# Optimization experiments

Measured on AMD Instinct MI355X. Metric: run time of the kernel, lower is better.

Reference implementation:

```python
import jax, jax.numpy as jnp
import numpy as np

N = 16384          # number of nodes
FEAT = 256         # in_features
POOL_RATIO = 0.5
K = max(2, int(POOL_RATIO * N))  # 8192, static


def setup_inputs() -> dict:
    key = jax.random.key(0)
    k1, k2, k3 = jax.random.split(key, 3)
    x = jax.random.normal(k1, (N, FEAT), dtype=jnp.float32)
    # dense proxy for the adjacency matrix (source calls A.todense())
    A = jax.random.uniform(k2, (N, N), dtype=jnp.float32)
    # fc: Linear(FEAT, 1, bias=None) -> weight vector of shape [FEAT]
    W = jax.random.normal(k3, (FEAT,), dtype=jnp.float32) * (1.0 / np.sqrt(FEAT))
    return {"x": x, "A": A, "W": W}


def reference(x, A, W):
    # score = fc(dropout(x)); dropout p=0 -> identity
    score = x @ W                                   # [N]
    # global L2 normalization: score / sqrt(sum(score**2))
    score = score / jnp.sqrt(jnp.sum(score * score))
    score = jnp.tanh(score)                         # activation_gPool
    values, idx = jax.lax.top_k(score, K)           # [K], [K]
    new_x = x[idx, :] * values[:, None]             # gather + scale  [K, FEAT]
    new_A = A[idx, :][:, idx]                       # [K, K] subgraph adjacency
    return new_x, new_A, idx
```

## Files before the change

kernel.cpp:

```cpp
#include <hip/hip_runtime.h>
#include <hip/hip_bf16.h>

#define N     16384
#define FEAT  256
#define KSEL  8192
#define NCHUNK 16
#define CHUNK (N / NCHUNK)

typedef float f32x4 __attribute__((ext_vector_type(4)));

__device__ __align__(16) double             g_s[N];
__device__ __align__(16) unsigned long long g_key[N];
__device__ __align__(16) int                g_cnt[N];
__device__ __align__(16) int                g_sel[KSEL];
__device__ __align__(16) float              g_vals[KSEL];
__device__              double              g_norminv;

static __device__ __forceinline__ unsigned long long mono_key(double s) {
    unsigned long long u = (unsigned long long)__double_as_longlong(s);
    if (u & 0x8000000000000000ull) u = ~u;
    else                           u |= 0x8000000000000000ull;
    return u;
}

__global__ __launch_bounds__(512) void k_score(const float* __restrict__ x,
                                               const float* __restrict__ W) {
    int lane = threadIdx.x & 63;
    int row  = blockIdx.x * 8 + (threadIdx.x >> 6);
    float4 xv = reinterpret_cast<const float4*>(x)[row * 64 + lane];
    float4 wv = reinterpret_cast<const float4*>(W)[lane];
    double acc = (double)xv.x * (double)wv.x + (double)xv.y * (double)wv.y
               + (double)xv.z * (double)wv.z + (double)xv.w * (double)wv.w;
    #pragma unroll
    for (int m = 32; m >= 1; m >>= 1) acc += __shfl_xor(acc, m, 64);
    if (lane == 0) { g_s[row] = acc; g_key[row] = mono_key(acc); g_cnt[row] = 0; }
}

__global__ __launch_bounds__(256) void k_rank() {
    __shared__ unsigned long long lk[CHUNK];
    int i = blockIdx.x * 256 + threadIdx.x;
    int jbase = blockIdx.y * CHUNK;
    for (int t = threadIdx.x; t < CHUNK; t += 256) lk[t] = g_key[jbase + t];
    __syncthreads();
    unsigned long long ki = g_key[i];
    int c = 0;
    #pragma unroll 8
    for (int jj = 0; jj < CHUNK; ++jj) {
        unsigned long long kj = lk[jj];
        c += (int)((kj > ki) | ((kj == ki) & ((jbase + jj) < i)));
    }
    atomicAdd(&g_cnt[i], c);

    if (blockIdx.x == 0 && blockIdx.y == 0) {
        __shared__ double red[256];
        double acc = 0.0;
        for (int j = threadIdx.x; j < N; j += 256) { double v = g_s[j]; acc += v * v; }
        red[threadIdx.x] = acc;
        __syncthreads();
        for (int w = 128; w >= 1; w >>= 1) {
            if ((int)threadIdx.x < w) red[threadIdx.x] += red[threadIdx.x + w];
            __syncthreads();
        }
        if (threadIdx.x == 0) g_norminv = 1.0 / sqrt(red[0]);
    }
}

__global__ void k_select(float* __restrict__ out_idx) {
    int i = blockIdx.x * 256 + threadIdx.x;
    int r = g_cnt[i];
    if ((unsigned)r < (unsigned)KSEL) {
        g_sel[r]   = i;
        g_vals[r]  = tanhf((float)(g_s[i] * g_norminv));
        out_idx[r] = (float)i;
    }
}

__global__ __launch_bounds__(512) void k_gather(const float* __restrict__ x,
                                                const float* __restrict__ A,
                                                f32x4* __restrict__ outx,
                                                f32x4* __restrict__ outA) {
    __shared__ unsigned short rowb[N];
    int r = blockIdx.x;
    int srcr = g_sel[r] & (N - 1);

    if (threadIdx.x < 64) {
        float v = g_vals[r];
        f32x4 xv = reinterpret_cast<const f32x4*>(x + (size_t)srcr * FEAT)[threadIdx.x];
        outx[(size_t)r * (FEAT / 4) + threadIdx.x] = xv * v;
    }

    const f32x4* src = reinterpret_cast<const f32x4*>(A + (size_t)srcr * N);
    uint2* rb = reinterpret_cast<uint2*>(rowb);
    #pragma unroll
    for (int it = 0; it < (N / 4) / 512; ++it) {
        int t = it * 512 + threadIdx.x;
        f32x4 a = __builtin_nontemporal_load(src + t);
        uint2 p;
        p.x = (__float_as_uint(a.y) & 0xFFFF0000u) | (__float_as_uint(a.x) >> 16);
        p.y = (__float_as_uint(a.w) & 0xFFFF0000u) | (__float_as_uint(a.z) >> 16);
        rb[t] = p;
    }
    __syncthreads();

    const int4* sel4 = reinterpret_cast<const int4*>(g_sel);
    #pragma unroll
    for (int it = 0; it < (KSEL / 4) / 512; ++it) {
        int c4 = it * 512 + threadIdx.x;
        int4 cc = sel4[c4];
        f32x4 o;
        o.x = __uint_as_float((unsigned)rowb[cc.x & (N - 1)] << 16);
        o.y = __uint_as_float((unsigned)rowb[cc.y & (N - 1)] << 16);
        o.z = __uint_as_float((unsigned)rowb[cc.z & (N - 1)] << 16);
        o.w = __uint_as_float((unsigned)rowb[cc.w & (N - 1)] << 16);
        __builtin_nontemporal_store(o, outA + (size_t)r * (KSEL / 4) + c4);
    }
}

extern "C" void kernel_launch(void* const* d_in, const int* in_sizes, int n_in,
                              void* d_out, int out_size, void* d_ws, size_t ws_size,
                              hipStream_t stream) {
    const float* x = nullptr; const float* A = nullptr; const float* W = nullptr;
    for (int i = 0; i < n_in; ++i) {
        if      (in_sizes[i] == N * FEAT) x = (const float*)d_in[i];
        else if (in_sizes[i] == N * N)    A = (const float*)d_in[i];
        else if (in_sizes[i] == FEAT)     W = (const float*)d_in[i];
    }
    if (!x || !A || !W) return;

    float* out = (float*)d_out;
    float* out_x   = out;
    float* out_A   = out + (size_t)KSEL * FEAT;
    float* out_idx = out + (size_t)out_size - KSEL;

    hipLaunchKernelGGL(k_score, dim3(N / 8), dim3(512), 0, stream, x, W);
    hipLaunchKernelGGL(k_rank, dim3(N / 256, NCHUNK), dim3(256), 0, stream);
    hipLaunchKernelGGL(k_select, dim3(N / 256), dim3(256), 0, stream, out_idx);
    hipLaunchKernelGGL(k_gather, dim3(KSEL), dim3(512), 0, stream,
                       x, A, (f32x4*)out_x, (f32x4*)out_A);
}
```

Before: 191.9 us.

## Double-buffer A rows in LDS and process multiple rows per gather block

The gather kernel now has each 1024-thread block handle 16 selected rows instead of one. Two LDS row buffers let the block issue global loads for the next A row while it gathers columns of the current row from the other buffer. The aim is to overlap the large streaming reads of A with the LDS-gather and store phase, and to cut per-block launch overhead. In exchange, each block uses 64KB of LDS and there are far fewer blocks, so fewer waves per CU are available to hide memory latency through occupancy.

```diff
diff --git a/kernel.cpp b/kernel.cpp
--- a/kernel.cpp
+++ b/kernel.cpp
@@ -6,6 +6,8 @@
 #define KSEL  8192
 #define NCHUNK 16
 #define CHUNK (N / NCHUNK)
+#define RPB   16
+#define GTHR  1024
 
 typedef float f32x4 __attribute__((ext_vector_type(4)));
 
@@ -75,44 +77,75 @@
     }
 }
 
-__global__ __launch_bounds__(512) void k_gather(const float* __restrict__ x,
-                                                const float* __restrict__ A,
-                                                f32x4* __restrict__ outx,
-                                                f32x4* __restrict__ outA) {
-    __shared__ unsigned short rowb[N];
-    int r = blockIdx.x;
-    int srcr = g_sel[r] & (N - 1);
+__global__ __launch_bounds__(GTHR) void k_gather(const float* __restrict__ x,
+                                                 const float* __restrict__ A,
+                                                 f32x4* __restrict__ outx,
+                                                 f32x4* __restrict__ outA) {
+    __shared__ unsigned short rowb[2][N];
+    const int tid  = threadIdx.x;
+    const int base = blockIdx.x * RPB;
 
-    if (threadIdx.x < 64) {
-        float v = g_vals[r];
-        f32x4 xv = reinterpret_cast<const f32x4*>(x + (size_t)srcr * FEAT)[threadIdx.x];
-        outx[(size_t)r * (FEAT / 4) + threadIdx.x] = xv * v;
+    {
+        int rr   = tid >> 6;
+        int lane = tid & 63;
+        int r    = base + rr;
+        int src  = g_sel[r] & (N - 1);
+        float v  = g_vals[r];
+        f32x4 xv = reinterpret_cast<const f32x4*>(x + (size_t)src * FEAT)[lane];
+        outx[(size_t)r * (FEAT / 4) + lane] = xv * v;
     }
 
-    const f32x4* src = reinterpret_cast<const f32x4*>(A + (size_t)srcr * N);
-    uint2* rb = reinterpret_cast<uint2*>(rowb);
-    #pragma unroll
-    for (int it = 0; it < (N / 4) / 512; ++it) {
-        int t = it * 512 + threadIdx.x;
-        f32x4 a = __builtin_nontemporal_load(src + t);
-        uint2 p;
-        p.x = (__float_as_uint(a.y) & 0xFFFF0000u) | (__float_as_uint(a.x) >> 16);
-        p.y = (__float_as_uint(a.w) & 0xFFFF0000u) | (__float_as_uint(a.z) >> 16);
-        rb[t] = p;
+    f32x4 st[4];
+    {
+        int src0 = g_sel[base] & (N - 1);
+        const f32x4* srcp = reinterpret_cast<const f32x4*>(A + (size_t)src0 * N);
+        #pragma unroll
+        for (int it = 0; it < 4; ++it)
+            st[it] = __builtin_nontemporal_load(srcp + it * GTHR + tid);
+        uint2* rb = reinterpret_cast<uint2*>(rowb[0]);
+        #pragma unroll
+        for (int it = 0; it < 4; ++it) {
+            uint2 p;
+            p.x = (__float_as_uint(st[it].y) & 0xFFFF0000u) | (__float_as_uint(st[it].x) >> 16);
+            p.y = (__float_as_uint(st[it].w) & 0xFFFF0000u) | (__float_as_uint(st[it].z) >> 16);
+            rb[it * GTHR + tid] = p;
+        }
     }
-    __syncthreads();
 
     const int4* sel4 = reinterpret_cast<const int4*>(g_sel);
-    #pragma unroll
-    for (int it = 0; it < (KSEL / 4) / 512; ++it) {
-        int c4 = it * 512 + threadIdx.x;
-        int4 cc = sel4[c4];
-        f32x4 o;
-        o.x = __uint_as_float((unsigned)rowb[cc.x & (N - 1)] << 16);
-        o.y = __uint_as_float((unsigned)rowb[cc.y & (N - 1)] << 16);
-        o.z = __uint_as_float((unsigned)rowb[cc.z & (N - 1)] << 16);
-        o.w = __uint_as_float((unsigned)rowb[cc.w & (N - 1)] << 16);
-        __builtin_nontemporal_store(o, outA + (size_t)r * (KSEL / 4) + c4);
+    #pragma unroll 1
+    for (int rr = 0; rr < RPB; ++rr) {
+        __syncthreads();
+        if (rr + 1 < RPB) {
+            int srcn = g_sel[base + rr + 1] & (N - 1);
+            const f32x4* srcp = reinterpret_cast<const f32x4*>(A + (size_t)srcn * N);
+            #pragma unroll
+            for (int it = 0; it < 4; ++it)
+                st[it] = __builtin_nontemporal_load(srcp + it * GTHR + tid);
+        }
+        const unsigned short* rb = rowb[rr & 1];
+        int r = base + rr;
+        #pragma unroll
+        for (int it = 0; it < (KSEL / 4) / GTHR; ++it) {
+            int c4 = it * GTHR + tid;
+            int4 cc = sel4[c4];
+            f32x4 o;
+            o.x = __uint_as_float((unsigned)rb[cc.x & (N - 1)] << 16);
+            o.y = __uint_as_float((unsigned)rb[cc.y & (N - 1)] << 16);
+            o.z = __uint_as_float((unsigned)rb[cc.z & (N - 1)] << 16);
+            o.w = __uint_as_float((unsigned)rb[cc.w & (N - 1)] << 16);
+            __builtin_nontemporal_store(o, outA + (size_t)r * (KSEL / 4) + c4);
+        }
+        if (rr + 1 < RPB) {
+            uint2* rbn = reinterpret_cast<uint2*>(rowb[(rr + 1) & 1]);
+            #pragma unroll
+            for (int it = 0; it < 4; ++it) {
+                uint2 p;
+                p.x = (__float_as_uint(st[it].y) & 0xFFFF0000u) | (__float_as_uint(st[it].x) >> 16);
+                p.y = (__float_as_uint(st[it].w) & 0xFFFF0000u) | (__float_as_uint(st[it].z) >> 16);
+                rbn[it * GTHR + tid] = p;
+            }
+        }
     }
 }
 
@@ -135,6 +168,6 @@
     hipLaunchKernelGGL(k_score, dim3(N / 8), dim3(512), 0, stream, x, W);
     hipLaunchKernelGGL(k_rank, dim3(N / 256, NCHUNK), dim3(256), 0, stream);
     hipLaunchKernelGGL(k_select, dim3(N / 256), dim3(256), 0, stream, out_idx);
-    hipLaunchKernelGGL(k_gather, dim3(KSEL), dim3(512), 0, stream,
+    hipLaunchKernelGGL(k_gather, dim3(KSEL / RPB), dim3(GTHR), 0, stream,
                        x, A, (f32x4*)out_x, (f32x4*)out_A);
 }
```

Result: slower. 201.6 us (+5.1%).

## Replace all-pairs rank with histogram bucketing and hoist gather row loads

Applied to the files above, without the earlier changes.

The O(N^2) pairwise rank kernel is replaced by four steps: a 15-bit key histogram built during scoring, a single-block scan, a scatter into buckets, and ranking within each bucket only. The L2 norm is also reworked into per-block partial sums that the scan kernel reduces, instead of one serial block. In the gather kernel, all eight row loads of A are issued up front, before the x-row work, so more memory requests are in flight. The risk is that the 15-bit bins are coarse for normally distributed scores, so a few buckets can be large and make ranking within them uneven and serial. The histogram also depends on the scatter pass decrementing it back to zero so the next call starts clean.

```diff
diff --git a/kernel.cpp b/kernel.cpp
--- a/kernel.cpp
+++ b/kernel.cpp
@@ -4,17 +4,19 @@
 #define N     16384
 #define FEAT  256
 #define KSEL  8192
-#define NCHUNK 16
-#define CHUNK (N / NCHUNK)
+#define NBIN  32768
 
 typedef float f32x4 __attribute__((ext_vector_type(4)));
 
-__device__ __align__(16) double             g_s[N];
+__device__ __align__(16) double   g_s[N];
 __device__ __align__(16) unsigned long long g_key[N];
-__device__ __align__(16) int                g_cnt[N];
-__device__ __align__(16) int                g_sel[KSEL];
-__device__ __align__(16) float              g_vals[KSEL];
-__device__              double              g_norminv;
+__device__ __align__(16) double   g_part[2048];
+__device__ __align__(16) unsigned g_hist[NBIN];
+__device__ __align__(16) unsigned g_hist2[NBIN];
+__device__ __align__(16) int      g_bucket[N];
+__device__ __align__(16) int      g_sel[KSEL];
+__device__ __align__(16) float    g_vals[KSEL];
+__device__              double    g_norminv;
 
 static __device__ __forceinline__ unsigned long long mono_key(double s) {
     unsigned long long u = (unsigned long long)__double_as_longlong(s);
@@ -25,50 +27,85 @@
 
 __global__ __launch_bounds__(512) void k_score(const float* __restrict__ x,
                                                const float* __restrict__ W) {
+    __shared__ double s_p[8];
     int lane = threadIdx.x & 63;
-    int row  = blockIdx.x * 8 + (threadIdx.x >> 6);
+    int wv   = threadIdx.x >> 6;
+    int row  = blockIdx.x * 8 + wv;
     float4 xv = reinterpret_cast<const float4*>(x)[row * 64 + lane];
-    float4 wv = reinterpret_cast<const float4*>(W)[lane];
-    double acc = (double)xv.x * (double)wv.x + (double)xv.y * (double)wv.y
-               + (double)xv.z * (double)wv.z + (double)xv.w * (double)wv.w;
+    float4 wvec = reinterpret_cast<const float4*>(W)[lane];
+    double acc = (double)xv.x * (double)wvec.x + (double)xv.y * (double)wvec.y
+               + (double)xv.z * (double)wvec.z + (double)xv.w * (double)wvec.w;
     #pragma unroll
     for (int m = 32; m >= 1; m >>= 1) acc += __shfl_xor(acc, m, 64);
-    if (lane == 0) { g_s[row] = acc; g_key[row] = mono_key(acc); g_cnt[row] = 0; }
-}
-
-__global__ __launch_bounds__(256) void k_rank() {
-    __shared__ unsigned long long lk[CHUNK];
-    int i = blockIdx.x * 256 + threadIdx.x;
-    int jbase = blockIdx.y * CHUNK;
-    for (int t = threadIdx.x; t < CHUNK; t += 256) lk[t] = g_key[jbase + t];
+    if (lane == 0) {
+        unsigned long long k = mono_key(acc);
+        g_s[row]   = acc;
+        g_key[row] = k;
+        atomicAdd(&g_hist[(unsigned)(k >> 49)], 1u);
+        s_p[wv] = acc * acc;
+    }
     __syncthreads();
-    unsigned long long ki = g_key[i];
-    int c = 0;
-    #pragma unroll 8
-    for (int jj = 0; jj < CHUNK; ++jj) {
-        unsigned long long kj = lk[jj];
-        c += (int)((kj > ki) | ((kj == ki) & ((jbase + jj) < i)));
-    }
-    atomicAdd(&g_cnt[i], c);
-
-    if (blockIdx.x == 0 && blockIdx.y == 0) {
-        __shared__ double red[256];
-        double acc = 0.0;
-        for (int j = threadIdx.x; j < N; j += 256) { double v = g_s[j]; acc += v * v; }
-        red[threadIdx.x] = acc;
-        __syncthreads();
-        for (int w = 128; w >= 1; w >>= 1) {
-            if ((int)threadIdx.x < w) red[threadIdx.x] += red[threadIdx.x + w];
-            __syncthreads();
-        }
-        if (threadIdx.x == 0) g_norminv = 1.0 / sqrt(red[0]);
+    if (threadIdx.x == 0) {
+        double p = 0.0;
+        #pragma unroll
+        for (int k = 0; k < 8; ++k) p += s_p[k];
+        g_part[blockIdx.x] = p;
     }
 }
 
-__global__ void k_select(float* __restrict__ out_idx) {
+__global__ __launch_bounds__(1024) void k_scan() {
+    __shared__ double red[1024];
+    __shared__ unsigned Ts[1024];
+    const int t = threadIdx.x;
+
+    red[t] = g_part[t] + g_part[t + 1024];
+    __syncthreads();
+    for (int w = 512; w >= 1; w >>= 1) {
+        if (t < w) red[t] += red[t + w];
+        __syncthreads();
+    }
+    if (t == 0) g_norminv = 1.0 / sqrt(red[0]);
+
+    unsigned cnt[32]; unsigned S = 0;
+    #pragma unroll
+    for (int k = 0; k < 32; ++k) { cnt[k] = g_hist[t * 32 + k]; S += cnt[k]; }
+    Ts[t] = S;
+    __syncthreads();
+    for (int off = 1; off < 1024; off <<= 1) {
+        unsigned v = (t + off < 1024) ? Ts[t + off] : 0u;
+        __syncthreads();
+        Ts[t] += v;
+        __syncthreads();
+    }
+    unsigned running = Ts[t] - S;
+    #pragma unroll
+    for (int k = 31; k >= 0; --k) {
+        g_hist2[t * 32 + k] = running;
+        running += cnt[k];
+    }
+}
+
+__global__ __launch_bounds__(256) void k_scatter() {
     int i = blockIdx.x * 256 + threadIdx.x;
-    int r = g_cnt[i];
-    if ((unsigned)r < (unsigned)KSEL) {
+    unsigned bin = (unsigned)(g_key[i] >> 49);
+    int old = atomicSub((int*)&g_hist[bin], 1);
+    g_bucket[g_hist2[bin] + (unsigned)(old - 1)] = i;
+}
+
+__global__ __launch_bounds__(256) void k_ranksel(float* __restrict__ out_idx) {
+    int i = blockIdx.x * 256 + threadIdx.x;
+    unsigned long long ki = g_key[i];
+    unsigned bin = (unsigned)(ki >> 49);
+    unsigned base = g_hist2[bin];
+    unsigned cntb = (bin == 0 ? (unsigned)N : g_hist2[bin - 1]) - base;
+    unsigned c = 0;
+    for (unsigned m = 0; m < cntb; ++m) {
+        int j = g_bucket[base + m];
+        unsigned long long kj = g_key[j];
+        c += (unsigned)((kj > ki) | ((kj == ki) & (j < i)));
+    }
+    unsigned r = base + c;
+    if (r < (unsigned)KSEL) {
         g_sel[r]   = i;
         g_vals[r]  = tanhf((float)(g_s[i] * g_norminv));
         out_idx[r] = (float)i;
@@ -80,32 +117,36 @@
                                                 f32x4* __restrict__ outx,
                                                 f32x4* __restrict__ outA) {
     __shared__ unsigned short rowb[N];
+    const int tid = threadIdx.x;
     int r = blockIdx.x;
     int srcr = g_sel[r] & (N - 1);
 
-    if (threadIdx.x < 64) {
+    const f32x4* src = reinterpret_cast<const f32x4*>(A + (size_t)srcr * N);
+    f32x4 a[8];
+    #pragma unroll
+    for (int it = 0; it < 8; ++it)
+        a[it] = __builtin_nontemporal_load(src + it * 512 + tid);
+
+    if (tid < 64) {
         float v = g_vals[r];
-        f32x4 xv = reinterpret_cast<const f32x4*>(x + (size_t)srcr * FEAT)[threadIdx.x];
-        outx[(size_t)r * (FEAT / 4) + threadIdx.x] = xv * v;
+        f32x4 xv = reinterpret_cast<const f32x4*>(x + (size_t)srcr * FEAT)[tid];
+        outx[(size_t)r * (FEAT / 4) + tid] = xv * v;
     }
 
-    const f32x4* src = reinterpret_cast<const f32x4*>(A + (size_t)srcr * N);
     uint2* rb = reinterpret_cast<uint2*>(rowb);
     #pragma unroll
-    for (int it = 0; it < (N / 4) / 512; ++it) {
-        int t = it * 512 + threadIdx.x;
-        f32x4 a = __builtin_nontemporal_load(src + t);
+    for (int it = 0; it < 8; ++it) {
         uint2 p;
-        p.x = (__float_as_uint(a.y) & 0xFFFF0000u) | (__float_as_uint(a.x) >> 16);
-        p.y = (__float_as_uint(a.w) & 0xFFFF0000u) | (__float_as_uint(a.z) >> 16);
-        rb[t] = p;
+        p.x = (__float_as_uint(a[it].y) & 0xFFFF0000u) | (__float_as_uint(a[it].x) >> 16);
+        p.y = (__float_as_uint(a[it].w) & 0xFFFF0000u) | (__float_as_uint(a[it].z) >> 16);
+        rb[it * 512 + tid] = p;
     }
     __syncthreads();
 
     const int4* sel4 = reinterpret_cast<const int4*>(g_sel);
     #pragma unroll
     for (int it = 0; it < (KSEL / 4) / 512; ++it) {
-        int c4 = it * 512 + threadIdx.x;
+        int c4 = it * 512 + tid;
         int4 cc = sel4[c4];
         f32x4 o;
         o.x = __uint_as_float((unsigned)rowb[cc.x & (N - 1)] << 16);
@@ -132,9 +173,10 @@
     float* out_A   = out + (size_t)KSEL * FEAT;
     float* out_idx = out + (size_t)out_size - KSEL;
 
-    hipLaunchKernelGGL(k_score, dim3(N / 8), dim3(512), 0, stream, x, W);
-    hipLaunchKernelGGL(k_rank, dim3(N / 256, NCHUNK), dim3(256), 0, stream);
-    hipLaunchKernelGGL(k_select, dim3(N / 256), dim3(256), 0, stream, out_idx);
-    hipLaunchKernelGGL(k_gather, dim3(KSEL), dim3(512), 0, stream,
+    hipLaunchKernelGGL(k_score,   dim3(N / 8),  dim3(512),  0, stream, x, W);
+    hipLaunchKernelGGL(k_scan,    dim3(1),      dim3(1024), 0, stream);
+    hipLaunchKernelGGL(k_scatter, dim3(N / 256), dim3(256), 0, stream);
+    hipLaunchKernelGGL(k_ranksel, dim3(N / 256), dim3(256), 0, stream, out_idx);
+    hipLaunchKernelGGL(k_gather,  dim3(KSEL),   dim3(512),  0, stream,
                        x, A, (f32x4*)out_x, (f32x4*)out_A);
 }
```

Result: slower. 349.0 us (+81.9%).
